# Kernel tuning notes

Hardware: AMD Instinct MI355X
Metric: run time of the kernel (lower is better)

## Reference

```python
import jax, jax.numpy as jnp
import numpy as np

# CIM / quantization constants hardcoded in the source module
INPUT_BIT = 8
WEIGHT_BIT = 4
OUTPUT_BIT = 8
DAC_BIT = 2
ADC_BIT = 8
ADC_GAIN_1_SCALE = 1.0 / 63.0
GAIN_MIN, GAIN_MAX = 1.0, 255.0
N_SLICES = INPUT_BIT // DAC_BIT  # 4 bit-serial input slices of 2 bits each


def ste_round(v):
    # straight-through round: forward = round(v), backward = identity
    return v + jax.lax.stop_gradient(jnp.round(v) - v)


def conv2d(x, w):
    # NCHW conv, stride 1, padding k//2 (SAME for odd k)
    return jax.lax.conv_general_dilated(
        x, w, window_strides=(1, 1), padding='SAME',
        dimension_numbers=('NCHW', 'OIHW', 'NCHW'))


def setup_inputs() -> dict:
    key = jax.random.key(0)
    kx, kw, kb = jax.random.split(key, 3)
    B, Cin, H, W = 16, 4, 512, 512
    Cout, K = 8, 3
    x = jax.random.uniform(kx, (B, Cin, H, W), dtype=jnp.float32)  # non-negative activations
    weight = jax.random.normal(kw, (Cout, Cin, K, K), dtype=jnp.float32) * 0.05
    bias = jax.random.normal(kb, (Cout,), dtype=jnp.float32) * 0.01
    s_in = jnp.float32(1.0 / 255.0)   # LSQ input scale (8-bit unsigned)
    s_w = jnp.float32(0.02)           # LSQ weight scale (4-bit signed)
    s_out = jnp.float32(0.05)         # LSQ output scale (8-bit signed)
    return {"x": x, "weight": weight, "bias": bias,
            "s_in": s_in, "s_w": s_w, "s_out": s_out}


def reference(x, weight, bias, s_in, s_w, s_out):
    in_max = 2.0 ** INPUT_BIT - 1.0          # 255
    w_lim = 2.0 ** (WEIGHT_BIT - 1) - 1.0    # 7
    adc_max = 2.0 ** (ADC_BIT - 1) - 1.0     # 127
    o_lim = 2.0 ** (OUTPUT_BIT - 1) - 1.0    # 127
    base = float(2 ** DAC_BIT)               # 4 levels per DAC slice

    # LSQ quantization of input (unsigned) and weight (signed), STE rounding
    xq = jnp.clip(ste_round(x / s_in), 0.0, in_max)        # integer-valued floats
    wq = jnp.clip(ste_round(weight / s_w), -w_lim, w_lim)

    # ideal integer conv (gradient path)
    ideal = conv2d(xq, wq)

    # bit-serial DAC/ADC CIM path (forward only; noise_scale=0 so no noise)
    xi = jax.lax.stop_gradient(xq)
    wi = jax.lax.stop_gradient(wq)
    psums = []
    for s in range(N_SLICES):
        sl = jnp.mod(jnp.floor(xi / (base ** s)), base)    # 2-bit slice in [0,3]
        psums.append(conv2d(sl, wi))
    # ADC gain adjustment ('gain' mode): integer gain in [1,255], LSB = 1/(gain*gain_1_scale)
    p_absmax = jnp.maximum(
        jnp.max(jnp.stack([jnp.max(jnp.abs(p)) for p in psums])), 1e-6)
    gain = jnp.clip(jnp.round(adc_max / (p_absmax * ADC_GAIN_1_SCALE)),
                    GAIN_MIN, GAIN_MAX)
    step = 1.0 / (gain * ADC_GAIN_1_SCALE)
    acc = jnp.zeros_like(ideal)
    for s, p in enumerate(psums):
        adc_out = jnp.clip(jnp.round(p / step), -adc_max, adc_max) * step
        acc = acc + adc_out * (base ** s)

    # straight-through: forward uses analog path, backward uses ideal conv
    psum = ideal + jax.lax.stop_gradient(acc - ideal)

    out = psum * (s_in * s_w) + bias[None, :, None, None]
    # LSQ output quantization (8-bit signed)
    out = jnp.clip(ste_round(out / s_out), -o_lim, o_lim) * s_out
    return out
```

## Files before the change

### kernel.cpp

```cpp
#include <hip/hip_runtime.h>
#include <stdint.h>

#define B_   16
#define CIN  4
#define COUT 8
#define H_   512
#define W_   512
#define HP   (H_ + 2)
#define WP   (W_ + 2)
#define PMAX 756
#define TBL  (2 * PMAX + 1)
#define RPB  8
#define GY   (H_ / RPB)
#define NBLK (2 * GY * B_)
#define NQ   (B_ * HP)

__device__ __forceinline__ int dot4(uint32_t a, int b, int c) {
#if __has_builtin(__builtin_amdgcn_sdot4)
    return __builtin_amdgcn_sdot4((int)a, b, c, false);
#else
    int r = c;
#pragma unroll
    for (int i = 0; i < 4; ++i) {
        int av = (int)((a >> (8 * i)) & 0xFFu);
        int bv = ((int)(((uint32_t)b) << (24 - 8 * i))) >> 24;
        r += av * bv;
    }
    return r;
#endif
}

__device__ __forceinline__ int dot8(uint32_t a, int b, int c) {
#if __has_builtin(__builtin_amdgcn_sdot8)
    return __builtin_amdgcn_sdot8((int)a, b, c, false);
#else
    int r = c;
#pragma unroll
    for (int i = 0; i < 8; ++i) {
        int av = (int)((a >> (4 * i)) & 0xFu);
        int bv = ((int)(((uint32_t)b) << (28 - 4 * i))) >> 28;
        r += av * bv;
    }
    return r;
#endif
}

__device__ __forceinline__ float rfl_f(float v) {
    return __int_as_float(__builtin_amdgcn_readfirstlane(__float_as_int(v)));
}

__device__ __forceinline__ int wquant(const float* w, float s_w,
                                      int co, int ci, int tap) {
    const int kh = tap / 3, kw = tap % 3;
    float wv = w[((co * CIN + ci) * 3 + kh) * 3 + kw];
    float q  = rintf(__fdiv_rn(wv, s_w));
    q = fminf(fmaxf(q, -7.0f), 7.0f);
    return (int)q;
}

__global__ __launch_bounds__(128) void quant_pack_kernel(
        const float* __restrict__ x, const float* __restrict__ weight,
        const float* __restrict__ s_in_p, const float* __restrict__ s_w_p,
        uint32_t* __restrict__ xq, uint32_t* __restrict__ wq8) {
    const int raw = blockIdx.x;
    const int lin = (raw & 7) * (NQ / 8) + (raw >> 3);
    const int b = lin / HP, hp = lin % HP;
    const int t = threadIdx.x;
    if (raw == 0) {
        const float s_w = *s_w_p;
        if (t < 32) {
            const int co = t >> 2, p = t & 3;
            const int tA = (p == 0) ? 0 : (p == 1) ? 3 : (p == 2) ? 6 : 2;
            const int tB = (p == 0) ? 1 : (p == 1) ? 4 : (p == 2) ? 7 : 5;
            uint32_t v = 0;
#pragma unroll
            for (int ci = 0; ci < CIN; ++ci) {
                v |= ((uint32_t)(wquant(weight, s_w, co, ci, tA) & 0xF)) << (8 * ci);
                v |= ((uint32_t)(wquant(weight, s_w, co, ci, tB) & 0xF)) << (8 * ci + 4);
            }
            wq8[t] = v;
        } else if (t < 40) {
            const int co = t - 32;
            uint32_t v = 0;
#pragma unroll
            for (int ci = 0; ci < CIN; ++ci)
                v |= ((uint32_t)(wquant(weight, s_w, co, ci, 8) & 0xFF)) << (8 * ci);
            wq8[32 + co] = v;
        }
    }
    uint32_t* dst = xq + ((size_t)b * HP + hp) * WP;
    if (hp == 0 || hp == HP - 1) {
        for (int i = t; i < WP; i += 128) dst[i] = 0;
        return;
    }
    const float s_in = *s_in_p;
    const int h = hp - 1;
    const size_t plane = (size_t)H_ * W_;
    const float* xr = x + ((size_t)b * CIN) * plane + (size_t)h * W_ + 4 * t;
    float4 v0 = *(const float4*)(xr);
    float4 v1 = *(const float4*)(xr + plane);
    float4 v2 = *(const float4*)(xr + 2 * plane);
    float4 v3 = *(const float4*)(xr + 3 * plane);
    uint32_t o0 = 0, o1 = 0, o2 = 0, o3 = 0;
#define QP(f, ci, oj)                                                  \
    { float q = rintf(__fdiv_rn((f), s_in));                           \
      q = fminf(fmaxf(q, 0.0f), 255.0f);                               \
      oj |= ((uint32_t)(int)q) << (8 * (ci)); }
    QP(v0.x, 0, o0) QP(v0.y, 0, o1) QP(v0.z, 0, o2) QP(v0.w, 0, o3)
    QP(v1.x, 1, o0) QP(v1.y, 1, o1) QP(v1.z, 1, o2) QP(v1.w, 1, o3)
    QP(v2.x, 2, o0) QP(v2.y, 2, o1) QP(v2.z, 2, o2) QP(v2.w, 2, o3)
    QP(v3.x, 3, o0) QP(v3.y, 3, o1) QP(v3.z, 3, o2) QP(v3.w, 3, o3)
#undef QP
    uint32_t* d = dst + 1 + 4 * t;
    d[0] = o0; d[1] = o1; d[2] = o2; d[3] = o3;
    if (t == 0) dst[0] = 0;
    if (t == 127) dst[WP - 1] = 0;
}

#define LOADW()                                                              \
    int w8s[32], w4s[8];                                                     \
    {                                                                        \
        const int4* q4 = (const int4*)wq8;                                   \
        _Pragma("unroll")                                                    \
        for (int i = 0; i < 8; ++i) {                                        \
            int4 w4i = q4[i];                                                \
            w8s[4 * i + 0] = __builtin_amdgcn_readfirstlane(w4i.x);          \
            w8s[4 * i + 1] = __builtin_amdgcn_readfirstlane(w4i.y);          \
            w8s[4 * i + 2] = __builtin_amdgcn_readfirstlane(w4i.z);          \
            w8s[4 * i + 3] = __builtin_amdgcn_readfirstlane(w4i.w);          \
        }                                                                    \
        int4 a0 = q4[8], a1 = q4[9];                                         \
        w4s[0] = __builtin_amdgcn_readfirstlane(a0.x);                       \
        w4s[1] = __builtin_amdgcn_readfirstlane(a0.y);                       \
        w4s[2] = __builtin_amdgcn_readfirstlane(a0.z);                       \
        w4s[3] = __builtin_amdgcn_readfirstlane(a0.w);                       \
        w4s[4] = __builtin_amdgcn_readfirstlane(a1.x);                       \
        w4s[5] = __builtin_amdgcn_readfirstlane(a1.y);                       \
        w4s[6] = __builtin_amdgcn_readfirstlane(a1.z);                       \
        w4s[7] = __builtin_amdgcn_readfirstlane(a1.w);                       \
    }

#define SWZ()                                                                \
    const int raw = blockIdx.x;                                              \
    const int lin = (raw & 7) * (NBLK / 8) + (raw >> 3);                     \
    const int bx = lin & 1;                                                  \
    const int hy = (lin >> 1) & (GY - 1);                                    \
    const int b  = lin >> 7;                                                 \
    const int w0 = bx * 256 + threadIdx.x;                                   \
    const int h0 = hy * RPB;

#define EXTS(CA, SG, v0, v1, v2)                                             \
    do {                                                                     \
        uint32_t lo_ = ((v0) & 0x0F0F0F0Fu) | (((v1) << 4) & 0xF0F0F0F0u);   \
        uint32_t hi_ = (((v0) >> 4) & 0x0F0F0F0Fu) | ((v1) & 0xF0F0F0F0u);   \
        CA[0] = lo_ & 0x33333333u;                                           \
        CA[1] = (lo_ >> 2) & 0x33333333u;                                    \
        CA[2] = hi_ & 0x33333333u;                                           \
        CA[3] = (hi_ >> 2) & 0x33333333u;                                    \
        SG[0] = (v2)&0x03030303u;                                            \
        SG[1] = ((v2) >> 2) & 0x03030303u;                                   \
        SG[2] = ((v2) >> 4) & 0x03030303u;                                   \
        SG[3] = ((v2) >> 6) & 0x03030303u;                                   \
    } while (0)

#define RING_INIT()                                                          \
    uint32_t cA0[4], cA1[4], cA2[4], cA3[4];                                 \
    uint32_t sg0[4], sg1[4], sg2[4], sg3[4];                                 \
    {                                                                        \
        uint32_t r0 = base[0], r1 = base[1], r2 = base[2];                   \
        EXTS(cA0, sg0, r0, r1, r2);                                          \
        r0 = base[WP]; r1 = base[WP + 1]; r2 = base[WP + 2];                 \
        EXTS(cA1, sg1, r0, r1, r2);                                          \
    }                                                                        \
    uint32_t n0 = base[2 * WP], n1 = base[2 * WP + 1], n2 = base[2 * WP + 2];

#define PREF(S)                                                              \
    if ((S) < RPB - 1) {                                                     \
        const uint32_t* nr_ = base + (size_t)((S) + 3) * WP;                 \
        n0 = nr_[0]; n1 = nr_[1]; n2 = nr_[2];                               \
    }

#define DOTS(CAa, SGa, CAb, SGb, CAc, SGc, K, INIT, OUTV)                    \
    {                                                                        \
        int a_ = dot4(SGc[K], w4s[co], INIT);                                \
        a_ = dot8(CAa[K], w8s[co * 4 + 0], a_);                              \
        a_ = dot8(CAb[K], w8s[co * 4 + 1], a_);                              \
        a_ = dot8(CAc[K], w8s[co * 4 + 2], a_);                              \
        a_ = dot8(K == 0 ? pc0 : K == 1 ? pc1 : K == 2 ? pc2 : pc3,          \
                  w8s[co * 4 + 3], a_);                                      \
        OUTV = a_;                                                           \
    }

#define STEP1(S, CAa, SGa, CAb, SGb, CAc, SGc)                               \
    do {                                                                     \
        EXTS(CAc, SGc, n0, n1, n2);                                          \
        PREF(S);                                                             \
        const uint32_t pc0 = SGa[0] | (SGb[0] << 4);                         \
        const uint32_t pc1 = SGa[1] | (SGb[1] << 4);                         \
        const uint32_t pc2 = SGa[2] | (SGb[2] << 4);                         \
        const uint32_t pc3 = SGa[3] | (SGb[3] << 4);                         \
        _Pragma("unroll")                                                    \
        for (int co = 0; co < COUT; ++co) {                                  \
            int a0, a1, a2, a3;                                              \
            DOTS(CAa, SGa, CAb, SGb, CAc, SGc, 0, 0, a0);                    \
            DOTS(CAa, SGa, CAb, SGb, CAc, SGc, 1, 0, a1);                    \
            DOTS(CAa, SGa, CAb, SGb, CAc, SGc, 2, 0, a2);                    \
            DOTS(CAa, SGa, CAb, SGb, CAc, SGc, 3, 0, a3);                    \
            rMax0 = max(rMax0, a0); rMin0 = min(rMin0, a0);                  \
            rMax1 = max(rMax1, a1); rMin1 = min(rMin1, a1);                  \
            rMax2 = max(rMax2, a2); rMin2 = min(rMin2, a2);                  \
            rMax3 = max(rMax3, a3); rMin3 = min(rMin3, a3);                  \
        }                                                                    \
    } while (0)

__global__ __launch_bounds__(256, 8) void conv_absmax(
        const uint32_t* __restrict__ xq, const uint32_t* __restrict__ wq8,
        int* __restrict__ blkmax) {
    __shared__ int red[4];
    LOADW();
    SWZ();
    const uint32_t* base = xq + ((size_t)b * HP + h0) * WP + w0;
    RING_INIT();
    int rMax0 = 0, rMax1 = 0, rMax2 = 0, rMax3 = 0;
    int rMin0 = 0, rMin1 = 0, rMin2 = 0, rMin3 = 0;
    STEP1(0, cA0, sg0, cA1, sg1, cA2, sg2);
    STEP1(1, cA1, sg1, cA2, sg2, cA3, sg3);
    STEP1(2, cA2, sg2, cA3, sg3, cA0, sg0);
    STEP1(3, cA3, sg3, cA0, sg0, cA1, sg1);
    STEP1(4, cA0, sg0, cA1, sg1, cA2, sg2);
    STEP1(5, cA1, sg1, cA2, sg2, cA3, sg3);
    STEP1(6, cA2, sg2, cA3, sg3, cA0, sg0);
    STEP1(7, cA3, sg3, cA0, sg0, cA1, sg1);
    int m = max(max(max(rMax0, -rMin0), max(rMax1, -rMin1)),
                max(max(rMax2, -rMin2), max(rMax3, -rMin3)));
#pragma unroll
    for (int off = 1; off < 64; off <<= 1)
        m = max(m, __shfl_xor(m, off));
    if ((threadIdx.x & 63) == 0) red[threadIdx.x >> 6] = m;
    __syncthreads();
    if (threadIdx.x == 0)
        blkmax[raw] = max(max(red[0], red[1]), max(red[2], red[3]));
}

__global__ __launch_bounds__(256) void reduce_absmax(
        const int* __restrict__ blkmax, int* __restrict__ absmax) {
    __shared__ int red[4];
    const int t = threadIdx.x;
    int m = 0;
#pragma unroll
    for (int i = 0; i < NBLK / 256; ++i) m = max(m, blkmax[t + 256 * i]);
#pragma unroll
    for (int off = 1; off < 64; off <<= 1)
        m = max(m, __shfl_xor(m, off));
    if ((t & 63) == 0) red[t >> 6] = m;
    __syncthreads();
    if (t == 0)
        *absmax = max(max(red[0], red[1]), max(red[2], red[3]));
}

#define STEP2(S, CAa, SGa, CAb, SGb, CAc, SGc)                               \
    do {                                                                     \
        EXTS(CAc, SGc, n0, n1, n2);                                          \
        PREF(S);                                                             \
        const uint32_t pc0 = SGa[0] | (SGb[0] << 4);                         \
        const uint32_t pc1 = SGa[1] | (SGb[1] << 4);                         \
        const uint32_t pc2 = SGa[2] | (SGb[2] << 4);                         \
        const uint32_t pc3 = SGa[3] | (SGb[3] << 4);                         \
        int ax[COUT][4];                                                     \
        _Pragma("unroll")                                                    \
        for (int co = 0; co < COUT; ++co) {                                  \
            DOTS(CAa, SGa, CAb, SGb, CAc, SGc, 0, PMAX, ax[co][0]);          \
            DOTS(CAa, SGa, CAb, SGb, CAc, SGc, 1, PMAX, ax[co][1]);          \
            DOTS(CAa, SGa, CAb, SGb, CAc, SGc, 2, PMAX, ax[co][2]);          \
            DOTS(CAa, SGa, CAb, SGb, CAc, SGc, 3, PMAX, ax[co][3]);          \
        }                                                                    \
        float tv[COUT][4];                                                   \
        _Pragma("unroll")                                                    \
        for (int co = 0; co < COUT; ++co) {                                  \
            tv[co][0] = T0[ax[co][0]];                                       \
            tv[co][1] = T4[ax[co][1]];                                       \
            tv[co][2] = T0[ax[co][2]];                                       \
            tv[co][3] = T4[ax[co][3]];                                       \
        }                                                                    \
        float* orow = out + ((size_t)b * COUT * H_ + (size_t)(h0 + (S))) * W_ + w0; \
        _Pragma("unroll")                                                    \
        for (int co = 0; co < COUT; ++co) {                                  \
            float of = __fadd_rn(tv[co][0], tv[co][1]);                      \
            of = __fadd_rn(of, __fmul_rn(tv[co][2], 16.0f));                 \
            of = __fadd_rn(of, __fmul_rn(tv[co][3], 16.0f));                 \
            float o_ = __fadd_rn(__fmul_rn(of, scale), br[co]);              \
            float q0 = __fmul_rn(o_, y1);        \
            float rr = fmaf(-s_out, q0, o_);                                 \
            float qd = fmaf(rr, y1, q0);                                     \
            float q_ = rintf(qd);                                            \
            q_ = fminf(fmaxf(q_, -127.0f), 127.0f);                          \
            orow[(size_t)co * plane] = __fmul_rn(q_, s_out);                 \
        }                                                                    \
    } while (0)

__global__ __launch_bounds__(256) void conv_out(
        const uint32_t* __restrict__ xq, const uint32_t* __restrict__ wq8,
        const float* __restrict__ bias, const float* __restrict__ sp_in,
        const float* __restrict__ sp_w, const float* __restrict__ sp_out,
        const int* __restrict__ absmax, float* __restrict__ out) {
    __shared__ float T0[TBL];
    __shared__ float T4[TBL];
    LOADW();
    const float pabs = fmaxf((float)(*absmax), 1e-6f);
    const float c63  = 1.0f / 63.0f;
    float g = rintf(__fdiv_rn(127.0f, __fmul_rn(pabs, c63)));
    g = fminf(fmaxf(g, 1.0f), 255.0f);
    const float step = __fdiv_rn(1.0f, __fmul_rn(g, c63));
    for (int i = threadIdx.x; i < TBL; i += 256) {
        float p = (float)(i - PMAX);
        float r = rintf(__fdiv_rn(p, step));
        r = fminf(fmaxf(r, -127.0f), 127.0f);
        float v = __fmul_rn(r, step);
        T0[i] = v;
        T4[i] = 4.0f * v;
    }
    const float scale = __fmul_rn(rfl_f(*sp_in), rfl_f(*sp_w));
    const float s_out = rfl_f(*sp_out);
    float y0 = __builtin_amdgcn_rcpf(s_out);
    float e  = fmaf(-s_out, y0, 1.0f);
    const float y1 = fmaf(y0, e, y0);
    float br[COUT];
#pragma unroll
    for (int co = 0; co < COUT; ++co) br[co] = rfl_f(bias[co]);
    __syncthreads();

    SWZ();
    const uint32_t* base = xq + ((size_t)b * HP + h0) * WP + w0;
    const size_t plane = (size_t)H_ * W_;
    RING_INIT();
    STEP2(0, cA0, sg0, cA1, sg1, cA2, sg2);
    STEP2(1, cA1, sg1, cA2, sg2, cA3, sg3);
    STEP2(2, cA2, sg2, cA3, sg3, cA0, sg0);
    STEP2(3, cA3, sg3, cA0, sg0, cA1, sg1);
    STEP2(4, cA0, sg0, cA1, sg1, cA2, sg2);
    STEP2(5, cA1, sg1, cA2, sg2, cA3, sg3);
    STEP2(6, cA2, sg2, cA3, sg3, cA0, sg0);
    STEP2(7, cA3, sg3, cA0, sg0, cA1, sg1);
}

extern "C" void kernel_launch(void* const* d_in, const int* in_sizes, int n_in,
                              void* d_out, int out_size, void* d_ws, size_t ws_size,
                              hipStream_t stream) {
    const float* x      = (const float*)d_in[0];
    const float* weight = (const float*)d_in[1];
    const float* bias   = (const float*)d_in[2];
    const float* s_in   = (const float*)d_in[3];
    const float* s_w    = (const float*)d_in[4];
    const float* s_out  = (const float*)d_in[5];
    float* out = (float*)d_out;

    int*      absmax = (int*)d_ws;
    uint32_t* wq8    = (uint32_t*)((char*)d_ws + 256);
    int*      blkmax = (int*)((char*)d_ws + 1024);
    uint32_t* xq     = (uint32_t*)((char*)d_ws + 16384);

    quant_pack_kernel<<<dim3(NQ), dim3(128), 0, stream>>>(
        x, weight, s_in, s_w, xq, wq8);

    conv_absmax<<<dim3(NBLK), dim3(256), 0, stream>>>(xq, wq8, blkmax);

    reduce_absmax<<<dim3(1), dim3(256), 0, stream>>>(blkmax, absmax);

    conv_out<<<dim3(NBLK), dim3(256), 0, stream>>>(
        xq, wq8, bias, s_in, s_w, s_out, absmax, out);
}
```

Before: 92.97 us.

## Use reciprocal-multiply input quantization, drop weight readfirstlane, relax launch bounds

Input quantization now multiplies by a precomputed reciprocal with one FMA correction step instead of calling a full IEEE divide per element. The readfirstlane calls on the weight loads are removed, which may let the compiler keep the weights in vector registers rather than forcing them into scalar registers. Both conv kernels now declare a minimum of 2 blocks per multiprocessor (conv_absmax was previously 8), giving the compiler a larger register budget at the cost of occupancy. The reciprocal division may round differently from a true divide in rare cases.

Measured after the change: 92.78 us. Within noise of the previous version (-0.2%).

```diff
diff --git a/kernel.cpp b/kernel.cpp
--- a/kernel.cpp
+++ b/kernel.cpp
@@ -47,6 +47,16 @@
 
 __device__ __forceinline__ float rfl_f(float v) {
     return __int_as_float(__builtin_amdgcn_readfirstlane(__float_as_int(v)));
+}
+__device__ __forceinline__ float recip1(float d) {
+    float y0 = __builtin_amdgcn_rcpf(d);
+    float e  = fmaf(-d, y0, 1.0f);
+    return fmaf(y0, e, y0);
+}
+__device__ __forceinline__ float mdiv(float n, float d, float y) {
+    float q0 = __fmul_rn(n, y);
+    float rr = fmaf(-d, q0, n);
+    return fmaf(rr, y, q0);
 }
 
 __device__ __forceinline__ int wquant(const float* w, float s_w,
@@ -94,6 +104,7 @@
         return;
     }
     const float s_in = *s_in_p;
+    const float yin  = recip1(s_in);
     const int h = hp - 1;
     const size_t plane = (size_t)H_ * W_;
     const float* xr = x + ((size_t)b * CIN) * plane + (size_t)h * W_ + 4 * t;
@@ -103,7 +114,7 @@
     float4 v3 = *(const float4*)(xr + 3 * plane);
     uint32_t o0 = 0, o1 = 0, o2 = 0, o3 = 0;
 #define QP(f, ci, oj)                                                  \
-    { float q = rintf(__fdiv_rn((f), s_in));                           \
+    { float q = rintf(mdiv((f), s_in, yin));                           \
       q = fminf(fmaxf(q, 0.0f), 255.0f);                               \
       oj |= ((uint32_t)(int)q) << (8 * (ci)); }
     QP(v0.x, 0, o0) QP(v0.y, 0, o1) QP(v0.z, 0, o2) QP(v0.w, 0, o3)
@@ -124,20 +135,14 @@
         _Pragma("unroll")                                                    \
         for (int i = 0; i < 8; ++i) {                                        \
             int4 w4i = q4[i];                                                \
-            w8s[4 * i + 0] = __builtin_amdgcn_readfirstlane(w4i.x);          \
-            w8s[4 * i + 1] = __builtin_amdgcn_readfirstlane(w4i.y);          \
-            w8s[4 * i + 2] = __builtin_amdgcn_readfirstlane(w4i.z);          \
-            w8s[4 * i + 3] = __builtin_amdgcn_readfirstlane(w4i.w);          \
+            w8s[4 * i + 0] = w4i.x;                                          \
+            w8s[4 * i + 1] = w4i.y;                                          \
+            w8s[4 * i + 2] = w4i.z;                                          \
+            w8s[4 * i + 3] = w4i.w;                                          \
         }                                                                    \
         int4 a0 = q4[8], a1 = q4[9];                                         \
-        w4s[0] = __builtin_amdgcn_readfirstlane(a0.x);                       \
-        w4s[1] = __builtin_amdgcn_readfirstlane(a0.y);                       \
-        w4s[2] = __builtin_amdgcn_readfirstlane(a0.z);                       \
-        w4s[3] = __builtin_amdgcn_readfirstlane(a0.w);                       \
-        w4s[4] = __builtin_amdgcn_readfirstlane(a1.x);                       \
-        w4s[5] = __builtin_amdgcn_readfirstlane(a1.y);                       \
-        w4s[6] = __builtin_amdgcn_readfirstlane(a1.z);                       \
-        w4s[7] = __builtin_amdgcn_readfirstlane(a1.w);                       \
+        w4s[0] = a0.x; w4s[1] = a0.y; w4s[2] = a0.z; w4s[3] = a0.w;          \
+        w4s[4] = a1.x; w4s[5] = a1.y; w4s[6] = a1.z; w4s[7] = a1.w;          \
     }
 
 #define SWZ()                                                                \
@@ -213,7 +218,7 @@
         }                                                                    \
     } while (0)
 
-__global__ __launch_bounds__(256, 8) void conv_absmax(
+__global__ __launch_bounds__(256, 2) void conv_absmax(
         const uint32_t* __restrict__ xq, const uint32_t* __restrict__ wq8,
         int* __restrict__ blkmax) {
     __shared__ int red[4];
@@ -289,7 +294,7 @@
             of = __fadd_rn(of, __fmul_rn(tv[co][2], 16.0f));                 \
             of = __fadd_rn(of, __fmul_rn(tv[co][3], 16.0f));                 \
             float o_ = __fadd_rn(__fmul_rn(of, scale), br[co]);              \
-            float q0 = __fmul_rn(o_, y1);        \
+            float q0 = __fmul_rn(o_, y1);                                    \
             float rr = fmaf(-s_out, q0, o_);                                 \
             float qd = fmaf(rr, y1, q0);                                     \
             float q_ = rintf(qd);                                            \
@@ -298,7 +303,7 @@
         }                                                                    \
     } while (0)
 
-__global__ __launch_bounds__(256) void conv_out(
+__global__ __launch_bounds__(256, 2) void conv_out(
         const uint32_t* __restrict__ xq, const uint32_t* __restrict__ wq8,
         const float* __restrict__ bias, const float* __restrict__ sp_in,
         const float* __restrict__ sp_w, const float* __restrict__ sp_out,
@@ -321,9 +326,7 @@
     }
     const float scale = __fmul_rn(rfl_f(*sp_in), rfl_f(*sp_w));
     const float s_out = rfl_f(*sp_out);
-    float y0 = __builtin_amdgcn_rcpf(s_out);
-    float e  = fmaf(-s_out, y0, 1.0f);
-    const float y1 = fmaf(y0, e, y0);
+    const float y1    = recip1(s_out);
     float br[COUT];
 #pragma unroll
     for (int co = 0; co < COUT; ++co) br[co] = rfl_f(bias[co]);
```
